# Kernel optimization log

Hardware: AMD Instinct MI355X
Metric: run time of the kernel (lower is better)

## Reference

```python
import jax, jax.numpy as jnp
import numpy as np

N_NODES = 100000
N_EDGES = 1600000
D_IN = 128
HIDDEN = 64
N_CLASSES = 10
N_GRAPHS = 512


def setup_inputs() -> dict:
    key = jax.random.key(0)
    ks = jax.random.split(key, 9)
    x = jax.random.normal(ks[0], (N_NODES, D_IN), dtype=jnp.float32)
    edge_index = jax.random.randint(ks[1], (2, N_EDGES), 0, N_NODES, dtype=jnp.int32)
    batch = jnp.sort(jax.random.randint(ks[2], (N_NODES,), 0, N_GRAPHS, dtype=jnp.int32))
    # GCNConv: lin (no bias) + separate bias added after aggregation
    s1 = 1.0 / np.sqrt(D_IN)
    s2 = 1.0 / np.sqrt(HIDDEN)
    W1 = jax.random.uniform(ks[3], (D_IN, HIDDEN), jnp.float32, -s1, s1)
    b1 = jnp.zeros((HIDDEN,), jnp.float32)
    W2 = jax.random.uniform(ks[4], (HIDDEN, HIDDEN), jnp.float32, -s2, s2)
    b2 = jnp.zeros((HIDDEN,), jnp.float32)
    Wfc = jax.random.uniform(ks[5], (HIDDEN, N_CLASSES), jnp.float32, -s2, s2)
    bfc = jax.random.uniform(ks[6], (N_CLASSES,), jnp.float32, -s2, s2)
    return {"x": x, "edge_index": edge_index, "batch": batch,
            "W1": W1, "b1": b1, "W2": W2, "b2": b2, "Wfc": Wfc, "bfc": bfc}


def gcn_conv(x, src, dst, W, b, n_nodes):
    # symmetric normalization with added self-loops (PyG gcn_norm defaults)
    deg = jnp.zeros((n_nodes,), x.dtype).at[dst].add(1.0) + 1.0  # +1 self-loop
    dinv = jax.lax.rsqrt(deg)
    h = x @ W  # [N, out]
    coef = (dinv[src] * dinv[dst])[:, None]          # [E, 1]
    msg = h[src] * coef                               # [E, out]
    agg = jax.ops.segment_sum(msg, dst, num_segments=n_nodes)
    agg = agg + h * (dinv * dinv)[:, None]            # self-loop contribution
    return agg + b


def reference(x, edge_index, batch, W1, b1, W2, b2, Wfc, bfc):
    src, dst = edge_index[0], edge_index[1]
    n_nodes = x.shape[0]
    h = gcn_conv(x, src, dst, W1, b1, n_nodes)
    h = jax.nn.relu(h)
    # dropout skipped (inference, training=False)
    h = gcn_conv(h, src, dst, W2, b2, n_nodes)
    h = jax.nn.relu(h)
    # global mean pool over graphs
    sums = jax.ops.segment_sum(h, batch, num_segments=N_GRAPHS)
    cnts = jax.ops.segment_sum(jnp.ones((n_nodes,), h.dtype), batch, num_segments=N_GRAPHS)
    pooled = sums / jnp.maximum(cnts, 1.0)[:, None]   # [G, hidden]
    logits = pooled @ Wfc + bfc                        # [G, classes]
    return jax.nn.log_softmax(logits, axis=1)
```

## Files before the change

kernel.cpp:

```cpp
#include <hip/hip_runtime.h>
#include <cstdint>
#include <cstddef>

#define N_NODES   100000
#define N_EDGES   1600000
#define D_IN      128
#define HIDDEN    64
#define N_GRAPHS  512
#define N_CLASSES 10

#define NB   196
#define EB4  391
#define BCAP 12288
#define PSLOTS 8

typedef __attribute__((ext_vector_type(8))) short bf16x8;
typedef __attribute__((ext_vector_type(4))) float f32x4;
typedef __attribute__((ext_vector_type(2))) float f32x2;

__device__ inline float bf2f(unsigned short u) {
    return __uint_as_float(((unsigned int)u) << 16);
}
__device__ inline unsigned short f2bf(float f) {
    unsigned int x = __float_as_uint(f);
    return (unsigned short)((x + 0x7FFF + ((x >> 16) & 1)) >> 16);
}

__global__ __launch_bounds__(256)
void hist2_kernel(const int* __restrict__ dst, int* __restrict__ bucketTot) {
    __shared__ int cnt[NB];
    const int tid = threadIdx.x;
    for (int i = tid; i < NB; i += 256) cnt[i] = 0;
    __syncthreads();
    int base = blockIdx.x * 4096 + tid;
#pragma unroll
    for (int j = 0; j < 16; j++) {
        int t = base + j * 256;
        if (t < N_EDGES) atomicAdd(&cnt[dst[t] >> 9], 1);
    }
    __syncthreads();
    for (int b = tid; b < NB; b += 256) {
        int c = cnt[b];
        if (c) atomicAdd(&bucketTot[b], c);
    }
}

__global__ __launch_bounds__(256)
void scan196_kernel(const int* __restrict__ bucketTot, int* __restrict__ bucketBase,
                    int* __restrict__ bucketCur) {
    __shared__ int lds[256];
    int tid = threadIdx.x;
    int v = (tid < NB) ? bucketTot[tid] : 0;
    lds[tid] = v; __syncthreads();
    for (int off = 1; off < 256; off <<= 1) {
        int t = (tid >= off) ? lds[tid - off] : 0;
        __syncthreads();
        lds[tid] += t;
        __syncthreads();
    }
    int ex = lds[tid] - v;
    if (tid < NB) { bucketBase[tid] = ex; bucketCur[tid] = ex; }
    if (tid == 255) bucketBase[NB] = lds[255];
}

__global__ __launch_bounds__(256)
void scatter_kernel(const int* __restrict__ src, const int* __restrict__ dst,
                    int* __restrict__ bucketCur, unsigned int* __restrict__ edgeA) {
    __shared__ unsigned int epk[4096];
    __shared__ unsigned char ebk[4096];
    __shared__ int cnt[NB];
    __shared__ int off[NB];
    int tid = threadIdx.x, blk = blockIdx.x;
    for (int i = tid; i < NB; i += 256) cnt[i] = 0;
    __syncthreads();
    int base = blk * 4096;
#pragma unroll
    for (int j = 0; j < 16; j++) {
        int li = j * 256 + tid;
        int t = base + li;
        if (t < N_EDGES) {
            int d = dst[t];
            epk[li] = (((unsigned int)(d & 511)) << 17) | (unsigned int)src[t];
            ebk[li] = (unsigned char)(d >> 9);
            atomicAdd(&cnt[d >> 9], 1);
        }
    }
    __syncthreads();
    for (int b = tid; b < NB; b += 256) {
        int c = cnt[b];
        off[b] = c ? atomicAdd(&bucketCur[b], c) : 0;
    }
    __syncthreads();
    int nmax = min(4096, N_EDGES - base);
    for (int li = tid; li < nmax; li += 256) {
        int b = ebk[li];
        int r = atomicAdd(&off[b], 1);
        edgeA[r] = epk[li];
    }
}

__global__ __launch_bounds__(256)
void passB_kernel(const int* __restrict__ bucketBase, const unsigned int* __restrict__ edgeA,
                  int* __restrict__ noffs, float* __restrict__ dinv,
                  int* __restrict__ srcs2) {
    __shared__ int hist[512];
    __shared__ int off[512];
    __shared__ int ps[256];
    __shared__ unsigned int eds[BCAP];
    __shared__ int srcs_l[BCAP];

    int tid = threadIdx.x, b = blockIdx.x;
    int e0 = bucketBase[b];
    int e1 = bucketBase[b + 1];
    int n0 = b << 9;
    int nn = min(512, N_NODES - n0);
    int len = e1 - e0;

    hist[tid] = 0; hist[tid + 256] = 0;
    __syncthreads();
    if (len <= BCAP) {
        for (int i = tid; i < len; i += 256) {
            unsigned int e = edgeA[e0 + i];
            eds[i] = e;
            atomicAdd(&hist[e >> 17], 1);
        }
    } else {
        for (int i = tid; i < len; i += 256) atomicAdd(&hist[edgeA[e0 + i] >> 17], 1);
    }
    __syncthreads();

    for (int n = tid; n < nn; n += 256) dinv[n0 + n] = rsqrtf((float)hist[n] + 1.0f);

    int a0 = hist[2 * tid], a1 = hist[2 * tid + 1];
    ps[tid] = a0 + a1;
    __syncthreads();
    for (int d = 1; d < 256; d <<= 1) {
        int v = (tid >= d) ? ps[tid - d] : 0;
        __syncthreads();
        ps[tid] += v;
        __syncthreads();
    }
    int pre = ps[tid] - (a0 + a1);
    off[2 * tid] = pre;
    off[2 * tid + 1] = pre + a0;
    __syncthreads();

    for (int n = tid; n < nn; n += 256) noffs[n0 + n] = e0 + off[n];
    if (b == NB - 1 && tid == 0) noffs[N_NODES] = N_EDGES;
    __syncthreads();

    if (len <= BCAP) {
        for (int i = tid; i < len; i += 256) {
            unsigned int e = eds[i];
            int r = atomicAdd(&off[e >> 17], 1);
            srcs_l[r] = (int)(e & 0x1FFFFu);
        }
        __syncthreads();
        for (int i = tid; i < len; i += 256) srcs2[e0 + i] = srcs_l[i];
    } else {
        for (int i = tid; i < len; i += 256) {
            unsigned int e = edgeA[e0 + i];
            int r = atomicAdd(&off[e >> 17], 1);
            srcs2[e0 + r] = (int)(e & 0x1FFFFu);
        }
    }
}

__global__ __launch_bounds__(512)
void gemm1_kernel(const float* __restrict__ X, const float* __restrict__ W,
                  const float* __restrict__ dinv, unsigned short* __restrict__ H,
                  int n_rows) {
    constexpr int K  = D_IN;
    constexpr int KP = K + 8;
    __shared__ unsigned short Wt[64 * KP];

    const int tid  = threadIdx.x;
    const int row0 = blockIdx.x * 128;

    for (int i = tid; i < K * 64; i += 512) {
        int k = i >> 6;
        int n = i & 63;
        Wt[n * KP + k] = f2bf(W[i]);
    }

    const int wave = tid >> 6;
    const int lane = tid & 63;
    const int lrow = lane & 15;
    const int quad = lane >> 4;
    const int m = wave * 16 + lrow;
    const int row = row0 + m;
    const bool valid = row < n_rows;

    float4 xa[8];
    if (valid) {
        const float4* xr4 = (const float4*)(X + (size_t)row * K);
#pragma unroll
        for (int kt = 0; kt < 4; kt++) {
            int q = (kt * 32 + quad * 8) >> 2;
            xa[2 * kt]     = xr4[q];
            xa[2 * kt + 1] = xr4[q + 1];
        }
    } else {
#pragma unroll
        for (int j = 0; j < 8; j++) xa[j] = make_float4(0.f, 0.f, 0.f, 0.f);
    }
    __syncthreads();

    f32x4 acc0 = {0.f, 0.f, 0.f, 0.f};
    f32x4 acc1 = {0.f, 0.f, 0.f, 0.f};
    f32x4 acc2 = {0.f, 0.f, 0.f, 0.f};
    f32x4 acc3 = {0.f, 0.f, 0.f, 0.f};

#pragma unroll
    for (int kt = 0; kt < 4; kt++) {
        int k0 = kt * 32 + quad * 8;
        const float* f = (const float*)&xa[2 * kt];
        bf16x8 a;
#pragma unroll
        for (int j = 0; j < 8; j++) a[j] = (short)f2bf(f[j]);
        bf16x8 b0 = *(const bf16x8*)&Wt[(0 * 16 + lrow) * KP + k0];
        bf16x8 b1 = *(const bf16x8*)&Wt[(1 * 16 + lrow) * KP + k0];
        bf16x8 b2 = *(const bf16x8*)&Wt[(2 * 16 + lrow) * KP + k0];
        bf16x8 b3 = *(const bf16x8*)&Wt[(3 * 16 + lrow) * KP + k0];
        acc0 = __builtin_amdgcn_mfma_f32_16x16x32_bf16(a, b0, acc0, 0, 0, 0);
        acc1 = __builtin_amdgcn_mfma_f32_16x16x32_bf16(a, b1, acc1, 0, 0, 0);
        acc2 = __builtin_amdgcn_mfma_f32_16x16x32_bf16(a, b2, acc2, 0, 0, 0);
        acc3 = __builtin_amdgcn_mfma_f32_16x16x32_bf16(a, b3, acc3, 0, 0, 0);
    }

    f32x4 accs[4] = {acc0, acc1, acc2, acc3};
#pragma unroll
    for (int r = 0; r < 4; r++) {
        int orow = row0 + wave * 16 + quad * 4 + r;
        if (orow < n_rows) {
            float dv = dinv[orow];
#pragma unroll
            for (int c = 0; c < 4; c++)
                H[(size_t)orow * 64 + c * 16 + lrow] = f2bf(accs[c][r] * dv);
        }
    }
}

__device__ inline void upk_add(int4 u, float* acc) {
    unsigned int a = (unsigned int)u.x, b = (unsigned int)u.y;
    unsigned int d = (unsigned int)u.z, e = (unsigned int)u.w;
    acc[0] += __uint_as_float(a << 16);
    acc[1] += __uint_as_float(a & 0xFFFF0000u);
    acc[2] += __uint_as_float(b << 16);
    acc[3] += __uint_as_float(b & 0xFFFF0000u);
    acc[4] += __uint_as_float(d << 16);
    acc[5] += __uint_as_float(d & 0xFFFF0000u);
    acc[6] += __uint_as_float(e << 16);
    acc[7] += __uint_as_float(e & 0xFFFF0000u);
}

__device__ inline void upk8_add(int2 u, float* acc) {
    f32x2 p0 = __builtin_amdgcn_cvt_pk_f32_fp8(u.x, false);
    f32x2 p1 = __builtin_amdgcn_cvt_pk_f32_fp8(u.x, true);
    f32x2 p2 = __builtin_amdgcn_cvt_pk_f32_fp8(u.y, false);
    f32x2 p3 = __builtin_amdgcn_cvt_pk_f32_fp8(u.y, true);
    acc[0] += p0.x; acc[1] += p0.y;
    acc[2] += p1.x; acc[3] += p1.y;
    acc[4] += p2.x; acc[5] += p2.y;
    acc[6] += p3.x; acc[7] += p3.y;
}

__global__ __launch_bounds__(512)
void gather1_gemm2_kernel(const int* __restrict__ offs, const int* __restrict__ srcs,
                          const float* __restrict__ dinv, const unsigned short* __restrict__ h,
                          const float* __restrict__ b1v, const float* __restrict__ W2,
                          unsigned char* __restrict__ H8, int n_nodes) {
    constexpr int KP = 72;
    __shared__ unsigned short Hs[64 * KP];
    __shared__ unsigned short Wt[64 * KP];

    const int tid   = threadIdx.x;
    const int node0 = blockIdx.x * 64;

    for (int i = tid; i < 64 * 64; i += 512) {
        int k = i >> 6;
        int n = i & 63;
        Wt[n * KP + k] = f2bf(W2[i]);
    }

    const int g    = tid >> 3;
    const int node = node0 + g;
    const int cg   = (tid & 7) * 8;

    float acc[8];
#pragma unroll
    for (int j = 0; j < 8; j++) acc[j] = 0.f;
    float dn = 0.f;

    if (node < n_nodes) {
        dn = dinv[node];
        int4 us = *(const int4*)(h + (size_t)node * 64 + cg);
        upk_add(us, acc);

        int i = offs[node];
        const int i1 = offs[node + 1];
        int rem = i1 - i;
        if (rem > 0) {
            int s[16];
#pragma unroll
            for (int j = 0; j < 16; j++) s[j] = srcs[i + (j < rem ? j : rem - 1)];
            while (rem > 0) {
                int4 u16[16];
#pragma unroll
                for (int j = 0; j < 16; j++)
                    u16[j] = *(const int4*)(h + (size_t)s[j] * 64 + cg);
                const int cur  = rem < 16 ? rem : 16;
                const int ni   = i + cur;
                const int nrem = rem - cur;
                if (nrem > 0) {
#pragma unroll
                    for (int j = 0; j < 16; j++)
                        s[j] = srcs[ni + (j < nrem ? j : nrem - 1)];
                }
#pragma unroll
                for (int j = 0; j < 16; j++) { if (j < cur) upk_add(u16[j], acc); }
                i = ni; rem = nrem;
            }
        }
    }

    {
        float4 bv0 = *(const float4*)(b1v + cg);
        float4 bv1 = *(const float4*)(b1v + cg + 4);
        float r0 = fmaxf(dn * acc[0] + bv0.x, 0.f);
        float r1 = fmaxf(dn * acc[1] + bv0.y, 0.f);
        float r2 = fmaxf(dn * acc[2] + bv0.z, 0.f);
        float r3 = fmaxf(dn * acc[3] + bv0.w, 0.f);
        float r4 = fmaxf(dn * acc[4] + bv1.x, 0.f);
        float r5 = fmaxf(dn * acc[5] + bv1.y, 0.f);
        float r6 = fmaxf(dn * acc[6] + bv1.z, 0.f);
        float r7 = fmaxf(dn * acc[7] + bv1.w, 0.f);
        ushort4 p0 = make_ushort4(f2bf(r0), f2bf(r1), f2bf(r2), f2bf(r3));
        ushort4 p1 = make_ushort4(f2bf(r4), f2bf(r5), f2bf(r6), f2bf(r7));
        *(ushort4*)&Hs[g * KP + cg]     = p0;
        *(ushort4*)&Hs[g * KP + cg + 4] = p1;
    }
    __syncthreads();

    const int wave = tid >> 6;
    const int lane = tid & 63;
    const int lrow = lane & 15;
    const int quad = lane >> 4;
    const int rt = (wave & 3) * 16;
    const int ct = (wave >> 2) * 32;
    const int m = rt + lrow;

    f32x4 acc0 = {0.f, 0.f, 0.f, 0.f};
    f32x4 acc1 = {0.f, 0.f, 0.f, 0.f};
#pragma unroll
    for (int kt = 0; kt < 2; kt++) {
        int k0 = kt * 32 + quad * 8;
        bf16x8 a  = *(const bf16x8*)&Hs[m * KP + k0];
        bf16x8 w0 = *(const bf16x8*)&Wt[(ct + lrow) * KP + k0];
        bf16x8 w1 = *(const bf16x8*)&Wt[(ct + 16 + lrow) * KP + k0];
        acc0 = __builtin_amdgcn_mfma_f32_16x16x32_bf16(a, w0, acc0, 0, 0, 0);
        acc1 = __builtin_amdgcn_mfma_f32_16x16x32_bf16(a, w1, acc1, 0, 0, 0);
    }

    f32x4 accs[2] = {acc0, acc1};
#pragma unroll
    for (int r = 0; r < 4; r++) {
        int row = node0 + rt + quad * 4 + r;
        if (row < n_nodes) {
            float dv = dinv[row];
#pragma unroll
            for (int c = 0; c < 2; c++) {
                float v = accs[c][r] * dv;
                int p = __builtin_amdgcn_cvt_pk_fp8_f32(v, v, 0, false);
                H8[(size_t)row * 64 + ct + c * 16 + lrow] = (unsigned char)(p & 0xFF);
            }
        }
    }
}

__global__ __launch_bounds__(256)
void gather_fp8_pool_kernel(const int* __restrict__ offs, const int* __restrict__ srcs,
                            const float* __restrict__ dinv, const unsigned char* __restrict__ h8,
                            const float* __restrict__ b, const int* __restrict__ batch,
                            float* __restrict__ pooled, float* __restrict__ cnt,
                            int n_nodes) {
    __shared__ float pacc[PSLOTS][64];
    __shared__ float lcnt[PSLOTS];
    __shared__ int sg[2];

    int tid = threadIdx.x;
    int node0 = blockIdx.x * 32;
    int lastn = min(node0 + 31, n_nodes - 1);
    for (int i = tid; i < PSLOTS * 64; i += 256) ((float*)pacc)[i] = 0.f;
    if (tid < PSLOTS) lcnt[tid] = 0.f;
    if (tid == 0) { sg[0] = batch[min(node0, n_nodes - 1)]; sg[1] = batch[lastn]; }
    __syncthreads();
    int g0 = sg[0];
    bool single = (sg[0] == sg[1]);

    int node = node0 + (tid >> 3);
    int cg = (tid & 7) * 8;

    float r[8];
#pragma unroll
    for (int j = 0; j < 8; j++) r[j] = 0.f;

    if (node < n_nodes) {
        float dn = dinv[node];
        float acc[8];
#pragma unroll
        for (int j = 0; j < 8; j++) acc[j] = 0.f;
        {
            int2 u = *(const int2*)(h8 + (size_t)node * 64 + cg);
            upk8_add(u, acc);
        }

        int i = offs[node];
        const int i1 = offs[node + 1];
        int rem = i1 - i;
        if (rem > 0) {
            int s[16];
#pragma unroll
            for (int j = 0; j < 16; j++) s[j] = srcs[i + (j < rem ? j : rem - 1)];
            while (rem > 0) {
                int2 u16[16];
#pragma unroll
                for (int j = 0; j < 16; j++)
                    u16[j] = *(const int2*)(h8 + (size_t)s[j] * 64 + cg);
                const int cur  = rem < 16 ? rem : 16;
                const int ni   = i + cur;
                const int nrem = rem - cur;
                if (nrem > 0) {
#pragma unroll
                    for (int j = 0; j < 16; j++)
                        s[j] = srcs[ni + (j < nrem ? j : nrem - 1)];
                }
#pragma unroll
                for (int j = 0; j < 16; j++) { if (j < cur) upk8_add(u16[j], acc); }
                i = ni; rem = nrem;
            }
        }

        float4 b0 = *(const float4*)(b + cg);
        float4 b1 = *(const float4*)(b + cg + 4);
        r[0] = fmaxf(dn * acc[0] + b0.x, 0.f);
        r[1] = fmaxf(dn * acc[1] + b0.y, 0.f);
        r[2] = fmaxf(dn * acc[2] + b0.z, 0.f);
        r[3] = fmaxf(dn * acc[3] + b0.w, 0.f);
        r[4] = fmaxf(dn * acc[4] + b1.x, 0.f);
        r[5] = fmaxf(dn * acc[5] + b1.y, 0.f);
        r[6] = fmaxf(dn * acc[6] + b1.z, 0.f);
        r[7] = fmaxf(dn * acc[7] + b1.w, 0.f);
    }

    if (single) {
#pragma unroll
        for (int j = 0; j < 8; j++) {
            float v = r[j];
            v += __shfl_xor(v, 8);
            v += __shfl_xor(v, 16);
            v += __shfl_xor(v, 32);
            r[j] = v;
        }
        int wave = tid >> 6;
        int lane = tid & 63;
        if (lane < 8) {
#pragma unroll
            for (int j = 0; j < 8; j++) pacc[wave][lane * 8 + j] = r[j];
        }
        __syncthreads();
        if (tid < 64) {
            float s = pacc[0][tid] + pacc[1][tid] + pacc[2][tid] + pacc[3][tid];
            if (s != 0.f) unsafeAtomicAdd(&pooled[(size_t)g0 * 64 + tid], s);
        }
        if (tid == 0) {
            int valid = min(32, n_nodes - node0);
            unsafeAtomicAdd(&cnt[g0], (float)valid);
        }
    } else {
        if (node < n_nodes) {
            int g = batch[node];
            int slot = g - g0;
            if (slot < PSLOTS) {
#pragma unroll
                for (int j = 0; j < 8; j++) atomicAdd(&pacc[slot][cg + j], r[j]);
                if ((tid & 7) == 0) atomicAdd(&lcnt[slot], 1.f);
            } else {
#pragma unroll
                for (int j = 0; j < 8; j++) unsafeAtomicAdd(&pooled[(size_t)g * 64 + cg + j], r[j]);
                if ((tid & 7) == 0) unsafeAtomicAdd(&cnt[g], 1.f);
            }
        }
        __syncthreads();
        for (int i = tid; i < PSLOTS * 64; i += 256) {
            float v = ((float*)pacc)[i];
            if (v != 0.f) unsafeAtomicAdd(&pooled[(size_t)(g0 + (i >> 6)) * 64 + (i & 63)], v);
        }
        if (tid < PSLOTS && lcnt[tid] != 0.f) unsafeAtomicAdd(&cnt[g0 + tid], lcnt[tid]);
    }
}

__global__ __launch_bounds__(256)
void head_kernel(const float* __restrict__ pooled, const float* __restrict__ cnt,
                 const float* __restrict__ Wfc, const float* __restrict__ bfc,
                 float* __restrict__ out) {
    __shared__ float Ws[HIDDEN * N_CLASSES];
    __shared__ float bs[N_CLASSES];
    int tid = threadIdx.x;
    for (int i = tid; i < HIDDEN * N_CLASSES; i += 256) Ws[i] = Wfc[i];
    if (tid < N_CLASSES) bs[tid] = bfc[tid];
    __syncthreads();

    int g = blockIdx.x * 256 + tid;
    if (g >= N_GRAPHS) return;

    float inv = 1.f / fmaxf(cnt[g], 1.f);
    float p[HIDDEN];
#pragma unroll
    for (int k = 0; k < HIDDEN; k++) p[k] = pooled[(size_t)g * 64 + k] * inv;

    float lg[N_CLASSES];
    float m = -1e30f;
#pragma unroll
    for (int j = 0; j < N_CLASSES; j++) {
        float a = bs[j];
#pragma unroll
        for (int k = 0; k < HIDDEN; k++) a += p[k] * Ws[k * N_CLASSES + j];
        lg[j] = a;
        m = fmaxf(m, a);
    }
    float s = 0.f;
#pragma unroll
    for (int j = 0; j < N_CLASSES; j++) s += __expf(lg[j] - m);
    float lse = m + __logf(s);
#pragma unroll
    for (int j = 0; j < N_CLASSES; j++) out[(size_t)g * N_CLASSES + j] = lg[j] - lse;
}

extern "C" void kernel_launch(void* const* d_in, const int* in_sizes, int n_in,
                              void* d_out, int out_size, void* d_ws, size_t ws_size,
                              hipStream_t stream) {
    const float* x   = (const float*)d_in[0];
    const int*   ei  = (const int*)d_in[1];
    const int*   bat = (const int*)d_in[2];
    const float* W1  = (const float*)d_in[3];
    const float* b1  = (const float*)d_in[4];
    const float* W2  = (const float*)d_in[5];
    const float* b2  = (const float*)d_in[6];
    const float* Wfc = (const float*)d_in[7];
    const float* bfc = (const float*)d_in[8];
    float* out = (float*)d_out;

    const int* src = ei;
    const int* dst = ei + N_EDGES;

    char* ws = (char*)d_ws;

    const size_t OFF_H     = 0;
    const size_t OFF_SRCS2 = 12800000;
    const size_t OFF_NOFFS = 19200000;
    const size_t OFF_DINV  = 19600016;
    const size_t OFF_BUFB  = 25600000;
    const size_t OFF_EDGEA = 38400000;
    const size_t OFF_POOL  = 44800000;
    const size_t OFF_CNT   = 44931072;
    const size_t OFF_BTOT  = 44933120;
    const size_t OFF_BBASE = 44933904;
    const size_t OFF_BCUR  = 44934692;

    unsigned short* hbuf  = (unsigned short*)(ws + OFF_H);
    int*   srcs2  = (int*)  (ws + OFF_SRCS2);
    int*   noffs  = (int*)  (ws + OFF_NOFFS);
    float* dinv   = (float*)(ws + OFF_DINV);
    unsigned char* hbuf8 = (unsigned char*)(ws + OFF_BUFB);
    unsigned int* edgeA = (unsigned int*)(ws + OFF_EDGEA);
    float* pooled = (float*)(ws + OFF_POOL);
    float* cnt    = (float*)(ws + OFF_CNT);
    int* bucketTot  = (int*)(ws + OFF_BTOT);
    int* bucketBase = (int*)(ws + OFF_BBASE);
    int* bucketCur  = (int*)(ws + OFF_BCUR);

    const int GATHER_BLOCKS = (N_NODES * 8 + 255) / 256;
    const int GEMM2_BLOCKS = (N_NODES + 63) / 64;
    const int GEMM1_BLOCKS = (N_NODES + 127) / 128;

    hipMemsetAsync(pooled, 0, (size_t)(131072 + 2048 + 784), stream);

    hist2_kernel<<<EB4, 256, 0, stream>>>(dst, bucketTot);
    scan196_kernel<<<1, 256, 0, stream>>>(bucketTot, bucketBase, bucketCur);
    scatter_kernel<<<EB4, 256, 0, stream>>>(src, dst, bucketCur, edgeA);
    passB_kernel<<<NB, 256, 0, stream>>>(bucketBase, edgeA, noffs, dinv, srcs2);
    gemm1_kernel<<<GEMM1_BLOCKS, 512, 0, stream>>>(x, W1, dinv, hbuf, N_NODES);
    gather1_gemm2_kernel<<<GEMM2_BLOCKS, 512, 0, stream>>>(
        noffs, srcs2, dinv, hbuf, b1, W2, hbuf8, N_NODES);
    gather_fp8_pool_kernel<<<GATHER_BLOCKS, 256, 0, stream>>>(
        noffs, srcs2, dinv, hbuf8, b2, bat, pooled, cnt, N_NODES);

    head_kernel<<<(N_GRAPHS + 255) / 256, 256, 0, stream>>>(pooled, cnt, Wfc, bfc, out);
}
```

Baseline: 257.2 us.

## Shrink gather batches, double-buffer layer-2 gathers, drop LDS edge staging

In passB the shared-memory staging buffer for bucket edges is removed, so edges are re-read from global memory in the scatter pass; this halves LDS use and may raise occupancy. The layer-1 aggregation gathers 8 neighbors per batch instead of 16, which lowers register pressure. The layer-2 aggregation is rewritten as a two-stage software pipeline: the next 8 neighbor rows are loaded while the current 8 are accumulated. The costs are an extra global read of edges in passB and fewer loads in flight per step in layer 1.

```diff
diff --git a/kernel.cpp b/kernel.cpp
--- a/kernel.cpp
+++ b/kernel.cpp
@@ -106,7 +106,6 @@
     __shared__ int hist[512];
     __shared__ int off[512];
     __shared__ int ps[256];
-    __shared__ unsigned int eds[BCAP];
     __shared__ int srcs_l[BCAP];
 
     int tid = threadIdx.x, b = blockIdx.x;
@@ -118,15 +117,7 @@
 
     hist[tid] = 0; hist[tid + 256] = 0;
     __syncthreads();
-    if (len <= BCAP) {
-        for (int i = tid; i < len; i += 256) {
-            unsigned int e = edgeA[e0 + i];
-            eds[i] = e;
-            atomicAdd(&hist[e >> 17], 1);
-        }
-    } else {
-        for (int i = tid; i < len; i += 256) atomicAdd(&hist[edgeA[e0 + i] >> 17], 1);
-    }
+    for (int i = e0 + tid; i < e1; i += 256) atomicAdd(&hist[edgeA[i] >> 17], 1);
     __syncthreads();
 
     for (int n = tid; n < nn; n += 256) dinv[n0 + n] = rsqrtf((float)hist[n] + 1.0f);
@@ -150,16 +141,16 @@
     __syncthreads();
 
     if (len <= BCAP) {
-        for (int i = tid; i < len; i += 256) {
-            unsigned int e = eds[i];
+        for (int i = e0 + tid; i < e1; i += 256) {
+            unsigned int e = edgeA[i];
             int r = atomicAdd(&off[e >> 17], 1);
             srcs_l[r] = (int)(e & 0x1FFFFu);
         }
         __syncthreads();
         for (int i = tid; i < len; i += 256) srcs2[e0 + i] = srcs_l[i];
     } else {
-        for (int i = tid; i < len; i += 256) {
-            unsigned int e = edgeA[e0 + i];
+        for (int i = e0 + tid; i < e1; i += 256) {
+            unsigned int e = edgeA[i];
             int r = atomicAdd(&off[e >> 17], 1);
             srcs2[e0 + r] = (int)(e & 0x1FFFFu);
         }
@@ -301,24 +292,24 @@
         const int i1 = offs[node + 1];
         int rem = i1 - i;
         if (rem > 0) {
-            int s[16];
-#pragma unroll
-            for (int j = 0; j < 16; j++) s[j] = srcs[i + (j < rem ? j : rem - 1)];
+            int s[8];
+#pragma unroll
+            for (int j = 0; j < 8; j++) s[j] = srcs[i + (j < rem ? j : rem - 1)];
             while (rem > 0) {
-                int4 u16[16];
-#pragma unroll
-                for (int j = 0; j < 16; j++)
-                    u16[j] = *(const int4*)(h + (size_t)s[j] * 64 + cg);
-                const int cur  = rem < 16 ? rem : 16;
+                int4 u8[8];
+#pragma unroll
+                for (int j = 0; j < 8; j++)
+                    u8[j] = *(const int4*)(h + (size_t)s[j] * 64 + cg);
+                const int cur  = rem < 8 ? rem : 8;
                 const int ni   = i + cur;
                 const int nrem = rem - cur;
                 if (nrem > 0) {
 #pragma unroll
-                    for (int j = 0; j < 16; j++)
+                    for (int j = 0; j < 8; j++)
                         s[j] = srcs[ni + (j < nrem ? j : nrem - 1)];
                 }
 #pragma unroll
-                for (int j = 0; j < 16; j++) { if (j < cur) upk_add(u16[j], acc); }
+                for (int j = 0; j < 8; j++) { if (j < cur) upk_add(u8[j], acc); }
                 i = ni; rem = nrem;
             }
         }
@@ -418,27 +409,37 @@
         int i = offs[node];
         const int i1 = offs[node + 1];
         int rem = i1 - i;
+
+        int curA = 0;
+        int2 uA[8];
         if (rem > 0) {
-            int s[16];
-#pragma unroll
-            for (int j = 0; j < 16; j++) s[j] = srcs[i + (j < rem ? j : rem - 1)];
-            while (rem > 0) {
-                int2 u16[16];
-#pragma unroll
-                for (int j = 0; j < 16; j++)
-                    u16[j] = *(const int2*)(h8 + (size_t)s[j] * 64 + cg);
-                const int cur  = rem < 16 ? rem : 16;
-                const int ni   = i + cur;
-                const int nrem = rem - cur;
-                if (nrem > 0) {
-#pragma unroll
-                    for (int j = 0; j < 16; j++)
-                        s[j] = srcs[ni + (j < nrem ? j : nrem - 1)];
-                }
-#pragma unroll
-                for (int j = 0; j < 16; j++) { if (j < cur) upk8_add(u16[j], acc); }
-                i = ni; rem = nrem;
+            curA = rem < 8 ? rem : 8;
+            int sA[8];
+#pragma unroll
+            for (int j = 0; j < 8; j++) sA[j] = srcs[i + (j < curA ? j : curA - 1)];
+#pragma unroll
+            for (int j = 0; j < 8; j++)
+                uA[j] = *(const int2*)(h8 + (size_t)sA[j] * 64 + cg);
+            i += curA; rem -= curA;
+        }
+        while (curA > 0) {
+            int curB = 0;
+            int2 uB[8];
+            if (rem > 0) {
+                curB = rem < 8 ? rem : 8;
+                int sB[8];
+#pragma unroll
+                for (int j = 0; j < 8; j++) sB[j] = srcs[i + (j < curB ? j : curB - 1)];
+#pragma unroll
+                for (int j = 0; j < 8; j++)
+                    uB[j] = *(const int2*)(h8 + (size_t)sB[j] * 64 + cg);
+                i += curB; rem -= curB;
             }
+#pragma unroll
+            for (int j = 0; j < 8; j++) { if (j < curA) upk8_add(uA[j], acc); }
+#pragma unroll
+            for (int j = 0; j < 8; j++) uA[j] = uB[j];
+            curA = curB;
         }
 
         float4 b0 = *(const float4*)(b + cg);
```

After: 238.4 us. 1.08x faster.
